# Optimization experiments

Measured on AMD Instinct MI355X. Metric: run time of the kernel, lower is better.

Reference implementation:

```python
import jax, jax.numpy as jnp
import numpy as np

N_EMBD = 1024
HEAD_SIZE = 64

def setup_inputs() -> dict:
    key = jax.random.key(0)
    kx, kk, kq, kv = jax.random.split(key, 4)
    x = jax.random.normal(kx, (8, 2048, N_EMBD), dtype=jnp.float32)
    scale = 1.0 / np.sqrt(N_EMBD)
    # nn.Linear weights are [out, in]; kaiming-uniform-ish init
    Wk = jax.random.uniform(kk, (HEAD_SIZE, N_EMBD), dtype=jnp.float32, minval=-scale, maxval=scale)
    Wq = jax.random.uniform(kq, (HEAD_SIZE, N_EMBD), dtype=jnp.float32, minval=-scale, maxval=scale)
    Wv = jax.random.uniform(kv, (HEAD_SIZE, N_EMBD), dtype=jnp.float32, minval=-scale, maxval=scale)
    return {"x": x, "Wk": Wk, "Wq": Wq, "Wv": Wv}

def reference(x, Wk, Wq, Wv):
    # x: [B, T, E]; W*: [H, E] (torch Linear layout)
    k = jnp.einsum('bte,he->bth', x, Wk)
    q = jnp.einsum('bte,he->bth', x, Wq)
    v = jnp.einsum('bte,he->bth', x, Wv)
    inv_sqrt_h = 1.0 / np.sqrt(HEAD_SIZE)
    wei = jnp.einsum('bth,bsh->bts', q, k) * inv_sqrt_h  # [B, T, T]
    wei = jax.nn.softmax(wei, axis=-1)
    out = jnp.einsum('bts,bsh->bth', wei, v)  # [B, T, H]
    return out
```

## Files before the change

kernel.cpp:

```cpp
#include <hip/hip_runtime.h>
#include <cstdint>

#define NB 8
#define TS 2048
#define NE 1024
#define HD 64
#define MTOT (NB*TS)

typedef float     f4  __attribute__((ext_vector_type(4)));
typedef short     s8v __attribute__((ext_vector_type(8)));
typedef short     s4v __attribute__((ext_vector_type(4)));
typedef int       i4v __attribute__((ext_vector_type(4)));
typedef _Float16  h8  __attribute__((ext_vector_type(8)));

__device__ __forceinline__ short f2bf(float f) {
  union { float f; uint32_t u; } x; x.f = f;
  return (short)((x.u + 0x7FFFu + ((x.u >> 16) & 1u)) >> 16);
}

__device__ __forceinline__ int pack2(float lo, float hi) {
  union { float f; uint32_t u; } a, b; a.f = lo; b.f = hi;
  return (int)__builtin_amdgcn_perm(b.u + 0x8000u, a.u + 0x8000u, 0x07060302u);
}

__device__ __forceinline__ void gl2lds(const void* gptr, void* lptr) {
  auto g = (const __attribute__((address_space(1))) uint32_t*)gptr;
  auto l = (__attribute__((address_space(3))) uint32_t*)lptr;
  __builtin_amdgcn_global_load_lds(g, l, 16, 0, 0);
}

template <int N>
__device__ __forceinline__ void wait_barrier() {
  asm volatile("s_waitcnt vmcnt(%0) lgkmcnt(0)" :: "n"(N) : "memory");
  __builtin_amdgcn_s_barrier();
}

__global__ __launch_bounds__(256) void wconv_kernel(
    const float* __restrict__ Wk, const float* __restrict__ Wq, const float* __restrict__ Wv,
    short* __restrict__ wb)
{
  const int idx = (blockIdx.x * 256 + threadIdx.x) * 4;
  const int p = idx >> 16;
  const int off = idx & 65535;
  const float* W = (p == 0) ? Wq : (p == 1) ? Wk : Wv;
  const float s = (p == 0) ? 0.18033688011112042f : 1.0f;
  const float4 v = *(const float4*)&W[off];
  s4v h; h[0] = f2bf(v.x*s); h[1] = f2bf(v.y*s); h[2] = f2bf(v.z*s); h[3] = f2bf(v.w*s);
  *(s4v*)&wb[idx] = h;
}

__global__ __launch_bounds__(256) void proj_kernel(
    const float* __restrict__ x, const short* __restrict__ wb,
    short* __restrict__ qo, short* __restrict__ ko, _Float16* __restrict__ vo)
{
  __shared__ float Xs[4][32][64];
  __shared__ short Ws[2][192][64];
  const int tid = threadIdx.x;
  const int wv = tid >> 6, lane = tid & 63, n = lane & 15, quad = lane >> 4;
  const int mg = wv & 1, cg = wv >> 1;
  const int r0 = blockIdx.x * 32;
  const int xrow = lane >> 4, xslot = lane & 15;
  const int wrow = lane >> 3, wslot = lane & 7;

  auto dmaX = [&](int c, int buf) {
#pragma unroll
    for (int u = 0; u < 2; ++u) {
      const int R0 = (wv * 2 + u) * 4;
      const int row = R0 + xrow;
      const int gs = (xslot + row) & 15;
      gl2lds(&x[(size_t)(r0 + row) * NE + c * 64 + gs * 4], &Xs[buf][R0][0]);
    }
  };
  auto dmaW = [&](int c, int buf) {
#pragma unroll
    for (int u = 0; u < 6; ++u) {
      const int C0 = (wv * 6 + u) * 8;
      const int col = C0 + wrow;
      const int gs = (wslot + col) & 7;
      gl2lds(&wb[(size_t)col * NE + c * 64 + gs * 8], &Ws[buf][C0][0]);
    }
  };

  const f4 fz = {0.f, 0.f, 0.f, 0.f};
  f4 acc[6] = {fz, fz, fz, fz, fz, fz};

  auto compute = [&](int bw, int bx) {
    s8v a[2];
    const int row = mg * 16 + n;
#pragma unroll
    for (int kc = 0; kc < 2; ++kc) {
      const int u0 = kc * 8 + quad * 2;
      const float* pr = &Xs[bx][row][0];
      const f4 f0 = *(const f4*)(pr + (((u0    ) - row) & 15) * 4);
      const f4 f1 = *(const f4*)(pr + (((u0 + 1) - row) & 15) * 4);
      i4v ai;
      ai[0] = pack2(f0[0], f0[1]); ai[1] = pack2(f0[2], f0[3]);
      ai[2] = pack2(f1[0], f1[1]); ai[3] = pack2(f1[2], f1[3]);
      a[kc] = __builtin_bit_cast(s8v, ai);
    }
#pragma unroll
    for (int nf = 0; nf < 6; ++nf) {
      const int col = cg * 96 + nf * 16 + n;
      const s8v b0 = *(const s8v*)&Ws[bw][col][(((0 + quad) - col) & 7) * 8];
      const s8v b1 = *(const s8v*)&Ws[bw][col][(((4 + quad) - col) & 7) * 8];
      acc[nf] = __builtin_amdgcn_mfma_f32_16x16x32_bf16(a[0], b0, acc[nf], 0, 0, 0);
      acc[nf] = __builtin_amdgcn_mfma_f32_16x16x32_bf16(a[1], b1, acc[nf], 0, 0, 0);
    }
  };

  dmaW(0, 0); dmaX(0, 0); dmaX(1, 1); dmaX(2, 2);
  wait_barrier<4>();

  for (int t = 0; t < 16; ++t) {
    if (t <= 14) dmaW(t + 1, (t + 1) & 1);
    if (t <= 12) dmaX(t + 3, (t + 3) & 3);
    compute(t & 1, t & 3);
    if (t <= 12)      wait_barrier<2>();
    else if (t <= 14) wait_barrier<0>();
  }

#pragma unroll
  for (int nf = 0; nf < 6; ++nf) {
    const int gc = cg * 96 + nf * 16;
    const int p = gc >> 6;
    const int rcol = (gc & 63) + n;
#pragma unroll
    for (int i = 0; i < 4; ++i) {
      const int R = r0 + mg * 16 + quad * 4 + i;
      const float av = acc[nf][i];
      if (p == 0)      qo[(size_t)R * HD + rcol] = f2bf(av);
      else if (p == 1) ko[(size_t)R * HD + rcol] = f2bf(av);
      else {
        const int t2 = R & (TS - 1), b = t2 & 31;
        const int pos = (t2 & ~31) | (((b >> 2) & 3) << 3) | (((b >> 4) & 1) << 2) | (b & 3);
        vo[(size_t)(R >> 11) * HD * TS + (size_t)rcol * TS + pos] = (_Float16)av;
      }
    }
  }
}

__global__ __launch_bounds__(512) void attn_kernel(
    const short* __restrict__ q, const short* __restrict__ k,
    const _Float16* __restrict__ vT, float* __restrict__ out)
{
  __shared__ __align__(16) char smem[131072];
  const int tid = threadIdx.x;
  const int wv = tid >> 6, lane = tid & 63, n = lane & 15, quad = lane >> 4;
  const int kq = wv & 3, qg = wv >> 2;
  const int batch = blockIdx.x & 7;
  const int qgb = blockIdx.x >> 3;
  const int m0 = batch * TS + qgb * 64;
  const short*    kb = k  + (size_t)batch * TS * HD;
  const _Float16* vb = vT + (size_t)batch * HD * TS;
  const int drow = lane >> 3, dslot = lane & 7;
  const f4 fz = {0.f, 0.f, 0.f, 0.f};

  auto kbuf = [&](int buf) { return (short*)   (smem +         (kq * 2 + buf) * 8192); };
  auto vbuf = [&](int buf) { return (_Float16*)(smem + 65536 + (kq * 2 + buf) * 8192); };

  auto dmaKV = [&](int tt, int buf) {
    const int c = kq * 8 + tt;
#pragma unroll
    for (int u = 0; u < 4; ++u) {
      const int K0 = (qg * 4 + u) * 8;
      const int key = K0 + drow;
      const int gs = (dslot + key) & 7;
      gl2lds(&kb[(size_t)(c * 64 + key) * HD + gs * 8], kbuf(buf) + K0 * 64);
    }
#pragma unroll
    for (int u = 0; u < 4; ++u) {
      const int D0 = (qg * 4 + u) * 8;
      const int d = D0 + drow;
      const int gs = (dslot + d) & 7;
      gl2lds(&vb[(size_t)d * TS + c * 64 + gs * 8], vbuf(buf) + D0 * 64);
    }
  };

  s8v qf[2][2];
#pragma unroll
  for (int qh = 0; qh < 2; ++qh)
#pragma unroll
    for (int kc = 0; kc < 2; ++kc)
      qf[qh][kc] = *(const s8v*)&q[(size_t)(m0 + qg * 32 + qh * 16 + n) * HD + kc * 32 + quad * 8];

  f4 o[2][4] = {{fz, fz, fz, fz}, {fz, fz, fz, fz}};
  f4 lD[2] = {fz, fz};
  h8 ones;
#pragma unroll
  for (int j = 0; j < 8; ++j) ones[j] = (_Float16)1.0f;

  dmaKV(0, 0); dmaKV(1, 1);
  wait_barrier<8>();

  for (int t = 0; t < 8; ++t) {
    const int buf = t & 1;

    if (t >= 1 && t <= 6) dmaKV(t + 1, (t + 1) & 1);

    const short*    ks = kbuf(buf);
    const _Float16* vs = vbuf(buf);

    f4 st[2][4];
#pragma unroll
    for (int f = 0; f < 4; ++f) {
      const int key = f * 16 + n;
      const s8v k0 = *(const s8v*)&ks[key * 64 + (((0 + quad) - key) & 7) * 8];
      const s8v k1 = *(const s8v*)&ks[key * 64 + (((4 + quad) - key) & 7) * 8];
#pragma unroll
      for (int qh = 0; qh < 2; ++qh) {
        st[qh][f] = __builtin_amdgcn_mfma_f32_16x16x32_bf16(k0, qf[qh][0], fz, 0, 0, 0);
        st[qh][f] = __builtin_amdgcn_mfma_f32_16x16x32_bf16(k1, qf[qh][1], st[qh][f], 0, 0, 0);
      }
    }

    h8 pa[2][2];
#pragma unroll
    for (int qh = 0; qh < 2; ++qh)
#pragma unroll
      for (int pr = 0; pr < 2; ++pr)
#pragma unroll
        for (int hf = 0; hf < 2; ++hf)
#pragma unroll
          for (int i = 0; i < 4; ++i)
            pa[qh][pr][hf * 4 + i] = (_Float16)__builtin_amdgcn_exp2f(st[qh][pr * 2 + hf][i]);

#pragma unroll
    for (int pr = 0; pr < 2; ++pr) {
#pragma unroll
      for (int qh = 0; qh < 2; ++qh)
        lD[qh] = __builtin_amdgcn_mfma_f32_16x16x32_f16(pa[qh][pr], ones, lD[qh], 0, 0, 0);
#pragma unroll
      for (int g = 0; g < 4; ++g) {
        const int d = g * 16 + n;
        const h8 vf = *(const h8*)&vs[d * 64 + (((pr * 4 + quad) - d) & 7) * 8];
#pragma unroll
        for (int qh = 0; qh < 2; ++qh)
          o[qh][g] = __builtin_amdgcn_mfma_f32_16x16x32_f16(pa[qh][pr], vf, o[qh][g], 0, 0, 0);
      }
    }

    if (t <= 6) wait_barrier<0>();
  }

  __syncthreads();

  float* o_c = (float*)smem;
  float* l_c = (float*)(smem + 69632);
  if (n == 0)
#pragma unroll
    for (int qh = 0; qh < 2; ++qh)
#pragma unroll
      for (int i = 0; i < 4; ++i)
        l_c[kq * 64 + qg * 32 + qh * 16 + quad * 4 + i] = lD[qh][i];
#pragma unroll
  for (int qh = 0; qh < 2; ++qh)
#pragma unroll
    for (int g = 0; g < 4; ++g)
#pragma unroll
      for (int i = 0; i < 4; ++i)
        o_c[kq * 4352 + (qg * 32 + qh * 16 + quad * 4 + i) * 68 + g * 16 + n] = o[qh][g][i];
  __syncthreads();

#pragma unroll
  for (int rep = 0; rep < 2; ++rep) {
    const int idx = tid + rep * 512;
    const int qr = idx >> 4, d4 = (idx & 15) * 4;
    float L = 0.f;
    f4 r = fz;
#pragma unroll
    for (int c2 = 0; c2 < 4; ++c2) {
      L += l_c[c2 * 64 + qr];
      r += *(const f4*)&o_c[c2 * 4352 + qr * 68 + d4];
    }
    const float inv = 1.0f / L;
    r[0] *= inv; r[1] *= inv; r[2] *= inv; r[3] *= inv;
    *(f4*)&out[(size_t)(m0 + qr) * HD + d4] = r;
  }
}

extern "C" void kernel_launch(void* const* d_in, const int* in_sizes, int n_in,
                              void* d_out, int out_size, void* d_ws, size_t ws_size,
                              hipStream_t stream) {
  const float* x  = (const float*)d_in[0];
  const float* Wk = (const float*)d_in[1];
  const float* Wq = (const float*)d_in[2];
  const float* Wv = (const float*)d_in[3];
  float* out = (float*)d_out;

  short* qb = (short*)d_ws;
  short* kb = qb + (size_t)MTOT * HD;
  _Float16* vb = (_Float16*)(kb + (size_t)MTOT * HD);
  short* wb = (short*)(vb + (size_t)NB * HD * TS);

  wconv_kernel<<<192, 256, 0, stream>>>(Wk, Wq, Wv, wb);
  proj_kernel<<<MTOT / 32, 256, 0, stream>>>(x, wb, qb, kb, vb);
  attn_kernel<<<MTOT / 64, 512, 0, stream>>>(qb, kb, vb, out);
}
```

Before: 127.3 us.

## Split attention blocks to 32 queries with per-wave K/V tiles and no block barriers

The attention kernel shrinks each block from 512 threads and 64 queries to 256 threads and 32 queries, and doubles the grid. Each of the four waves now owns a private double-buffered K/V region in LDS. It streams 32-key tiles over its 512-key slice, waiting only on its own vmcnt instead of a block-wide barrier each iteration. This removes the inter-wave barrier stalls and halves LDS per block, so more blocks can fit per CU. In exchange, K/V tiles are no longer shared by two query groups, which doubles the global/L2 K/V traffic, and the smaller tiles add more loop iterations.

```diff
diff --git a/kernel.cpp b/kernel.cpp
--- a/kernel.cpp
+++ b/kernel.cpp
@@ -33,6 +33,11 @@
 __device__ __forceinline__ void wait_barrier() {
   asm volatile("s_waitcnt vmcnt(%0) lgkmcnt(0)" :: "n"(N) : "memory");
   __builtin_amdgcn_s_barrier();
+}
+
+template <int N>
+__device__ __forceinline__ void wave_wait() {
+  asm volatile("s_waitcnt vmcnt(%0)" :: "n"(N) : "memory");
 }
 
 __global__ __launch_bounds__(256) void wconv_kernel(
@@ -139,40 +144,41 @@
   }
 }
 
-__global__ __launch_bounds__(512) void attn_kernel(
+__global__ __launch_bounds__(256) void attn_kernel(
     const short* __restrict__ q, const short* __restrict__ k,
     const _Float16* __restrict__ vT, float* __restrict__ out)
 {
-  __shared__ __align__(16) char smem[131072];
+  __shared__ __align__(16) char smem[65536];
   const int tid = threadIdx.x;
   const int wv = tid >> 6, lane = tid & 63, n = lane & 15, quad = lane >> 4;
-  const int kq = wv & 3, qg = wv >> 2;
+  const int kq = wv;
   const int batch = blockIdx.x & 7;
   const int qgb = blockIdx.x >> 3;
-  const int m0 = batch * TS + qgb * 64;
+  const int m0 = batch * TS + qgb * 32;
   const short*    kb = k  + (size_t)batch * TS * HD;
   const _Float16* vb = vT + (size_t)batch * HD * TS;
-  const int drow = lane >> 3, dslot = lane & 7;
+  const int krow = lane >> 3, kslot = lane & 7;
+  const int vrow = lane >> 2, vslot = lane & 3;
   const f4 fz = {0.f, 0.f, 0.f, 0.f};
 
-  auto kbuf = [&](int buf) { return (short*)   (smem +         (kq * 2 + buf) * 8192); };
-  auto vbuf = [&](int buf) { return (_Float16*)(smem + 65536 + (kq * 2 + buf) * 8192); };
+  auto kbuf = [&](int buf) { return (short*)   (smem +         (kq * 2 + buf) * 4096); };
+  auto vbuf = [&](int buf) { return (_Float16*)(smem + 32768 + (kq * 2 + buf) * 4096); };
 
   auto dmaKV = [&](int tt, int buf) {
-    const int c = kq * 8 + tt;
+    const int c = kq * 16 + tt;
 #pragma unroll
     for (int u = 0; u < 4; ++u) {
-      const int K0 = (qg * 4 + u) * 8;
-      const int key = K0 + drow;
-      const int gs = (dslot + key) & 7;
-      gl2lds(&kb[(size_t)(c * 64 + key) * HD + gs * 8], kbuf(buf) + K0 * 64);
+      const int K0 = u * 8;
+      const int key = K0 + krow;
+      const int gs = (kslot + key) & 7;
+      gl2lds(&kb[(size_t)(c * 32 + key) * HD + gs * 8], kbuf(buf) + K0 * 64);
     }
 #pragma unroll
     for (int u = 0; u < 4; ++u) {
-      const int D0 = (qg * 4 + u) * 8;
-      const int d = D0 + drow;
-      const int gs = (dslot + d) & 7;
-      gl2lds(&vb[(size_t)d * TS + c * 64 + gs * 8], vbuf(buf) + D0 * 64);
+      const int D0 = u * 16;
+      const int d = D0 + vrow;
+      const int gs = (vslot + d) & 3;
+      gl2lds(&vb[(size_t)d * TS + c * 32 + gs * 8], vbuf(buf) + D0 * 32);
     }
   };
 
@@ -181,7 +187,7 @@
   for (int qh = 0; qh < 2; ++qh)
 #pragma unroll
     for (int kc = 0; kc < 2; ++kc)
-      qf[qh][kc] = *(const s8v*)&q[(size_t)(m0 + qg * 32 + qh * 16 + n) * HD + kc * 32 + quad * 8];
+      qf[qh][kc] = *(const s8v*)&q[(size_t)(m0 + qh * 16 + n) * HD + kc * 32 + quad * 8];
 
   f4 o[2][4] = {{fz, fz, fz, fz}, {fz, fz, fz, fz}};
   f4 lD[2] = {fz, fz};
@@ -190,19 +196,19 @@
   for (int j = 0; j < 8; ++j) ones[j] = (_Float16)1.0f;
 
   dmaKV(0, 0); dmaKV(1, 1);
-  wait_barrier<8>();
-
-  for (int t = 0; t < 8; ++t) {
+  wave_wait<8>();
+
+  for (int t = 0; t < 16; ++t) {
     const int buf = t & 1;
 
-    if (t >= 1 && t <= 6) dmaKV(t + 1, (t + 1) & 1);
+    if (t >= 1 && t <= 14) dmaKV(t + 1, (t + 1) & 1);
 
     const short*    ks = kbuf(buf);
     const _Float16* vs = vbuf(buf);
 
-    f4 st[2][4];
-#pragma unroll
-    for (int f = 0; f < 4; ++f) {
+    f4 st[2][2];
+#pragma unroll
+    for (int f = 0; f < 2; ++f) {
       const int key = f * 16 + n;
       const s8v k0 = *(const s8v*)&ks[key * 64 + (((0 + quad) - key) & 7) * 8];
       const s8v k1 = *(const s8v*)&ks[key * 64 + (((4 + quad) - key) & 7) * 8];
@@ -213,64 +219,59 @@
       }
     }
 
-    h8 pa[2][2];
+    h8 pa[2];
 #pragma unroll
     for (int qh = 0; qh < 2; ++qh)
 #pragma unroll
-      for (int pr = 0; pr < 2; ++pr)
-#pragma unroll
-        for (int hf = 0; hf < 2; ++hf)
-#pragma unroll
-          for (int i = 0; i < 4; ++i)
-            pa[qh][pr][hf * 4 + i] = (_Float16)__builtin_amdgcn_exp2f(st[qh][pr * 2 + hf][i]);
-
-#pragma unroll
-    for (int pr = 0; pr < 2; ++pr) {
+      for (int f = 0; f < 2; ++f)
+#pragma unroll
+        for (int i = 0; i < 4; ++i)
+          pa[qh][f * 4 + i] = (_Float16)__builtin_amdgcn_exp2f(st[qh][f][i]);
+
+#pragma unroll
+    for (int qh = 0; qh < 2; ++qh)
+      lD[qh] = __builtin_amdgcn_mfma_f32_16x16x32_f16(pa[qh], ones, lD[qh], 0, 0, 0);
+#pragma unroll
+    for (int g = 0; g < 4; ++g) {
+      const int d = g * 16 + n;
+      const h8 vf = *(const h8*)&vs[d * 32 + ((quad - d) & 3) * 8];
 #pragma unroll
       for (int qh = 0; qh < 2; ++qh)
-        lD[qh] = __builtin_amdgcn_mfma_f32_16x16x32_f16(pa[qh][pr], ones, lD[qh], 0, 0, 0);
-#pragma unroll
-      for (int g = 0; g < 4; ++g) {
-        const int d = g * 16 + n;
-        const h8 vf = *(const h8*)&vs[d * 64 + (((pr * 4 + quad) - d) & 7) * 8];
-#pragma unroll
-        for (int qh = 0; qh < 2; ++qh)
-          o[qh][g] = __builtin_amdgcn_mfma_f32_16x16x32_f16(pa[qh][pr], vf, o[qh][g], 0, 0, 0);
-      }
-    }
-
-    if (t <= 6) wait_barrier<0>();
+        o[qh][g] = __builtin_amdgcn_mfma_f32_16x16x32_f16(pa[qh], vf, o[qh][g], 0, 0, 0);
+    }
+
+    if (t <= 14) wave_wait<0>();
   }
 
   __syncthreads();
 
   float* o_c = (float*)smem;
-  float* l_c = (float*)(smem + 69632);
+  float* l_c = (float*)(smem + 34816);
   if (n == 0)
 #pragma unroll
     for (int qh = 0; qh < 2; ++qh)
 #pragma unroll
       for (int i = 0; i < 4; ++i)
-        l_c[kq * 64 + qg * 32 + qh * 16 + quad * 4 + i] = lD[qh][i];
+        l_c[kq * 32 + qh * 16 + quad * 4 + i] = lD[qh][i];
 #pragma unroll
   for (int qh = 0; qh < 2; ++qh)
 #pragma unroll
     for (int g = 0; g < 4; ++g)
 #pragma unroll
       for (int i = 0; i < 4; ++i)
-        o_c[kq * 4352 + (qg * 32 + qh * 16 + quad * 4 + i) * 68 + g * 16 + n] = o[qh][g][i];
+        o_c[kq * 2176 + (qh * 16 + quad * 4 + i) * 68 + g * 16 + n] = o[qh][g][i];
   __syncthreads();
 
 #pragma unroll
   for (int rep = 0; rep < 2; ++rep) {
-    const int idx = tid + rep * 512;
+    const int idx = tid + rep * 256;
     const int qr = idx >> 4, d4 = (idx & 15) * 4;
     float L = 0.f;
     f4 r = fz;
 #pragma unroll
     for (int c2 = 0; c2 < 4; ++c2) {
-      L += l_c[c2 * 64 + qr];
-      r += *(const f4*)&o_c[c2 * 4352 + qr * 68 + d4];
+      L += l_c[c2 * 32 + qr];
+      r += *(const f4*)&o_c[c2 * 2176 + qr * 68 + d4];
     }
     const float inv = 1.0f / L;
     r[0] *= inv; r[1] *= inv; r[2] *= inv; r[3] *= inv;
@@ -294,5 +295,5 @@
 
   wconv_kernel<<<192, 256, 0, stream>>>(Wk, Wq, Wv, wb);
   proj_kernel<<<MTOT / 32, 256, 0, stream>>>(x, wb, qb, kb, vb);
-  attn_kernel<<<MTOT / 64, 512, 0, stream>>>(qb, kb, vb, out);
-}
+  attn_kernel<<<MTOT / 32, 256, 0, stream>>>(qb, kb, vb, out);
+}
```

Result: slower. 131.5 us (+3.3%).
